# Kernel optimization log

Hardware: AMD Instinct MI355X
Metric: run time of the kernel (lower is better)

Reference implementation:

```python
import jax, jax.numpy as jnp
import numpy as np

B, L, E = 8, 512, 256
H = W = 128
NH = 8
HD = E // NH


def setup_inputs() -> dict:
    key = jax.random.key(0)
    ks = jax.random.split(key, 8)
    return {
        "query_row": jax.random.normal(ks[0], (B, L, E), jnp.float32),
        "query_col": jax.random.normal(ks[1], (B, L, E), jnp.float32),
        "key_row": jax.random.normal(ks[2], (B, H, W, E), jnp.float32),
        "key_col": jax.random.normal(ks[3], (B, H, W, E), jnp.float32),
        "value": jax.random.normal(ks[4], (B, H, W, E), jnp.float32),
        "in_proj_weight": jax.random.normal(ks[5], (5 * E, E), jnp.float32) * 0.02,
        "in_proj_bias": jnp.zeros((5 * E,), jnp.float32),
        "out_proj_weight": jax.random.normal(ks[6], (E, E), jnp.float32) * 0.02,
        "out_proj_bias": jnp.zeros((E,), jnp.float32),
    }


def reference(query_row, query_col, key_row, key_col, value,
              in_proj_weight, in_proj_bias, out_proj_weight, out_proj_bias):
    b, tgt_len, embed_dim = query_row.shape
    h, w = key_col.shape[1], key_row.shape[2]
    nh, hd = NH, embed_dim // NH
    scale = float(hd) ** -0.5

    def proj(x, i):
        Wi = in_proj_weight[i * embed_dim:(i + 1) * embed_dim]
        bi = in_proj_bias[i * embed_dim:(i + 1) * embed_dim]
        return x @ Wi.T + bi

    q_row = proj(query_row, 0) * scale            # [B,L,E]
    q_col = proj(query_col, 1) * scale            # [B,L,E]
    k_row = proj(key_row, 2).mean(axis=1)         # mean over H -> [B,W,E]
    k_col = proj(key_col, 3).mean(axis=2)         # mean over W -> [B,H,E]
    v = proj(value, 4)                            # [B,H,W,E]

    def heads(x):  # [..., E] -> [B, nh, ..., hd]
        return x.reshape(x.shape[:-1] + (nh, hd))

    q_row_h = heads(q_row).transpose(0, 2, 1, 3)        # [B,nh,L,hd]
    q_col_h = heads(q_col).transpose(0, 2, 1, 3)        # [B,nh,L,hd]
    k_row_h = heads(k_row).transpose(0, 2, 1, 3)        # [B,nh,W,hd]
    k_col_h = heads(k_col).transpose(0, 2, 1, 3)        # [B,nh,H,hd]
    v_h = heads(v).transpose(0, 3, 1, 2, 4)             # [B,nh,H,W,hd]

    a_row = jax.nn.softmax(jnp.einsum('bnld,bnwd->bnlw', q_row_h, k_row_h), axis=-1)
    a_col = jax.nn.softmax(jnp.einsum('bnld,bnhd->bnlh', q_col_h, k_col_h), axis=-1)

    # contract over H first, then over W (matches torch's src_len_col >= src_len_row branch)
    ao_col = jnp.einsum('bnlh,bnhwc->bnlwc', a_col, v_h)      # [B,nh,L,W,hd]
    out = jnp.einsum('bnlw,bnlwc->bnlc', a_row, ao_col)       # [B,nh,L,hd]

    out = out.transpose(2, 0, 1, 3).reshape(tgt_len, b, embed_dim)  # [L,B,E]
    return out @ out_proj_weight.T + out_proj_bias
```

## Files before the change

kernel.cpp:

```cpp
#include <hip/hip_runtime.h>
#include <stdint.h>

#define B_  8
#define L_  512
#define E_  256
#define H_  128
#define W_  128
#define NH_ 8
#define HD_ 32

typedef unsigned short ushort_t;
typedef __attribute__((ext_vector_type(8))) short bf16x8;
typedef __attribute__((ext_vector_type(4))) float f32x4;

__device__ __forceinline__ float bf2f(ushort_t u) {
    union { unsigned int i; float f; } x;
    x.i = ((unsigned int)u) << 16;
    return x.f;
}
__device__ __forceinline__ ushort_t f2bf(float f) {
    union { float f; unsigned int i; } x;
    x.f = f;
    unsigned int r = x.i + 0x7FFFu + ((x.i >> 16) & 1u);
    return (ushort_t)(r >> 16);
}

__global__ __launch_bounds__(256) void mean_h_kernel(const float* __restrict__ kr,
                                                     float* __restrict__ out) {
    int i = blockIdx.x * 256 + threadIdx.x;
    int e = i & (E_ - 1);
    int w = (i >> 8) & (W_ - 1);
    int b = i >> 15;
    const float* p = kr + ((size_t)b * H_ * W_ + w) * E_ + e;
    float s = 0.f;
#pragma unroll 8
    for (int h = 0; h < H_; ++h) s += p[(size_t)h * W_ * E_];
    out[i] = s * (1.0f / H_);
}
__global__ __launch_bounds__(256) void mean_w_kernel(const float* __restrict__ kc,
                                                     float* __restrict__ out) {
    int i = blockIdx.x * 256 + threadIdx.x;
    int e = i & (E_ - 1);
    int h = (i >> 8) & (H_ - 1);
    int b = i >> 15;
    const float* p = kc + ((size_t)(b * H_ + h) * W_) * E_ + e;
    float s = 0.f;
#pragma unroll 8
    for (int w = 0; w < W_; ++w) s += p[(size_t)w * E_];
    out[i] = s * (1.0f / W_);
}

__device__ __forceinline__ void load4f(const float* p, float* v) {
    float4 t = *(const float4*)p;
    v[0] = t.x; v[1] = t.y; v[2] = t.z; v[3] = t.w;
}
__device__ __forceinline__ void store4(float* p, float a, float b, float c, float d) {
    float4 t; t.x = a; t.y = b; t.z = c; t.w = d;
    *(float4*)p = t;
}

__global__ __launch_bounds__(256) void gemm256(const float* __restrict__ A,
                                               const float* __restrict__ Wt,
                                               const float* __restrict__ bias,
                                               float* __restrict__ C, int M, float scale) {
    __shared__ __align__(16) float As[16][64];
    __shared__ __align__(16) float Bs[16][64];
    const int m0 = blockIdx.x * 64;
    const int n0 = blockIdx.y * 64;
    const int tid = threadIdx.x;
    const int lr = tid >> 2;
    const int lk = (tid & 3) << 2;
    const int tx = tid & 15, ty = tid >> 4;
    float acc[4][4] = {{0.f}};

    for (int k0 = 0; k0 < E_; k0 += 16) {
        float av[4], wv[4];
        load4f(A + (size_t)(m0 + lr) * E_ + k0 + lk, av);
        load4f(Wt + (size_t)(n0 + lr) * E_ + k0 + lk, wv);
        As[lk + 0][lr] = av[0]; As[lk + 1][lr] = av[1];
        As[lk + 2][lr] = av[2]; As[lk + 3][lr] = av[3];
        Bs[lk + 0][lr] = wv[0]; Bs[lk + 1][lr] = wv[1];
        Bs[lk + 2][lr] = wv[2]; Bs[lk + 3][lr] = wv[3];
        __syncthreads();
#pragma unroll
        for (int k = 0; k < 16; ++k) {
            float a[4], b[4];
            load4f(&As[k][ty << 2], a);
            load4f(&Bs[k][tx << 2], b);
#pragma unroll
            for (int i = 0; i < 4; ++i)
#pragma unroll
                for (int j = 0; j < 4; ++j) acc[i][j] += a[i] * b[j];
        }
        __syncthreads();
    }
    float bv[4];
    load4f(bias + n0 + (tx << 2), bv);
#pragma unroll
    for (int i = 0; i < 4; ++i) {
        float* cp = C + (size_t)(m0 + (ty << 2) + i) * E_ + n0 + (tx << 2);
        store4(cp, scale * (acc[i][0] + bv[0]), scale * (acc[i][1] + bv[1]),
                   scale * (acc[i][2] + bv[2]), scale * (acc[i][3] + bv[3]));
    }
}

__global__ __launch_bounds__(256) void wconv_kernel(const float* __restrict__ w,
                                                    ushort_t* __restrict__ wbf) {
    int i = (blockIdx.x * 256 + threadIdx.x) * 4;
    float4 f = *(const float4*)(w + i);
    ushort4 u;
    u.x = f2bf(f.x); u.y = f2bf(f.y); u.z = f2bf(f.z); u.w = f2bf(f.w);
    *(ushort4*)(wbf + i) = u;
}

#define KP_ 264
__global__ __launch_bounds__(256, 3) void vproj_mfma(const float* __restrict__ Ag,
                                                     const ushort_t* __restrict__ Wbf,
                                                     const float* __restrict__ bias,
                                                     ushort_t* __restrict__ v_t) {
    __shared__ ushort_t A_lds[64 * KP_];
    const int m0 = blockIdx.x * 64;
    const int tid = threadIdx.x, lane = tid & 63, wv = tid >> 6;
    const int quad = lane >> 4, lc = lane & 15;
    {
        int r = tid >> 2, kq = (tid & 3) * 64;
        const float* sa = Ag + (size_t)(m0 + r) * 256 + kq;
        ushort_t* da = A_lds + r * KP_ + kq;
#pragma unroll
        for (int j = 0; j < 16; ++j) {
            float4 f = *(const float4*)(sa + j * 4);
            ushort4 u;
            u.x = f2bf(f.x); u.y = f2bf(f.y); u.z = f2bf(f.z); u.w = f2bf(f.w);
            *(ushort4*)(da + j * 4) = u;
        }
    }
    __syncthreads();

    f32x4 acc[4][4];
#pragma unroll
    for (int t = 0; t < 4; ++t)
#pragma unroll
        for (int et = 0; et < 4; ++et) {
            acc[t][et][0] = 0.f; acc[t][et][1] = 0.f;
            acc[t][et][2] = 0.f; acc[t][et][3] = 0.f;
        }

    const ushort_t* wrow = Wbf + (size_t)(wv * 64 + lc) * 256 + quad * 8;

    bf16x8 wf[4], wn[4];
#pragma unroll
    for (int et = 0; et < 4; ++et)
        wf[et] = *(const bf16x8*)(wrow + (size_t)(et * 16) * 256);

#pragma unroll
    for (int kc = 0; kc < 8; ++kc) {
        bf16x8 vf[4];
#pragma unroll
        for (int t = 0; t < 4; ++t)
            vf[t] = *(const bf16x8*)(A_lds + (t * 16 + lc) * KP_ + kc * 32 + quad * 8);
        if (kc < 7) {
#pragma unroll
            for (int et = 0; et < 4; ++et)
                wn[et] = *(const bf16x8*)(wrow + (size_t)(et * 16) * 256 + (kc + 1) * 32);
        }
#pragma unroll
        for (int et = 0; et < 4; ++et)
#pragma unroll
            for (int t = 0; t < 4; ++t)
                acc[t][et] = __builtin_amdgcn_mfma_f32_16x16x32_bf16(vf[t], wf[et], acc[t][et], 0, 0, 0);
#pragma unroll
        for (int et = 0; et < 4; ++et) wf[et] = wn[et];
    }

    const int b = m0 >> 14;
    const int ml = m0 & 16383;
    ushort_t* vtb = v_t + (size_t)b * 4194304 + ml + quad * 4;
#pragma unroll
    for (int et = 0; et < 4; ++et) {
        const int e = wv * 64 + et * 16 + lc;
        const float bv = bias[e];
        ushort_t* vte = vtb + (size_t)e * 16384;
#pragma unroll
        for (int t = 0; t < 4; ++t) {
            ushort4 u;
            u.x = f2bf(acc[t][et][0] + bv);
            u.y = f2bf(acc[t][et][1] + bv);
            u.z = f2bf(acc[t][et][2] + bv);
            u.w = f2bf(acc[t][et][3] + bv);
            *(ushort4*)(vte + t * 16) = u;
        }
    }
}

__global__ __launch_bounds__(256) void scores_row(const float* __restrict__ q,
                                                  const float* __restrict__ k,
                                                  float* __restrict__ a) {
    const int lt = blockIdx.x, bn = blockIdx.y;
    const int n = bn & 7, b = bn >> 3;
    const int tid = threadIdx.x;
    __shared__ float ks[128][36];
    {
        int r = tid >> 1, c16 = (tid & 1) * 16;
        const float* src = k + ((size_t)b * 128 + r) * 256 + n * 32 + c16;
#pragma unroll
        for (int j = 0; j < 4; ++j) {
            float4 f = *(const float4*)(src + j * 4);
            ks[r][c16 + j * 4 + 0] = f.x; ks[r][c16 + j * 4 + 1] = f.y;
            ks[r][c16 + j * 4 + 2] = f.z; ks[r][c16 + j * 4 + 3] = f.w;
        }
    }
    const int ll = tid >> 3, wq = tid & 7;
    float4 q4r[8];
    {
        const float* qp = q + ((size_t)b * 512 + lt * 32 + ll) * 256 + n * 32;
#pragma unroll
        for (int c4 = 0; c4 < 8; ++c4) q4r[c4] = *(const float4*)(qp + c4 * 4);
    }
    __syncthreads();
    float dots[16];
#pragma unroll
    for (int j = 0; j < 16; ++j) dots[j] = 0.f;
#pragma unroll
    for (int c4 = 0; c4 < 8; ++c4) {
        float4 q4 = q4r[c4];
#pragma unroll
        for (int j = 0; j < 16; ++j) {
            float4 k4 = *(const float4*)&ks[j * 8 + wq][c4 * 4];
            dots[j] += q4.x * k4.x + q4.y * k4.y + q4.z * k4.z + q4.w * k4.w;
        }
    }
    float mx = dots[0];
#pragma unroll
    for (int j = 1; j < 16; ++j) mx = fmaxf(mx, dots[j]);
    for (int d = 1; d < 8; d <<= 1) mx = fmaxf(mx, __shfl_xor(mx, d, 64));
    float ex[16], sm = 0.f;
#pragma unroll
    for (int j = 0; j < 16; ++j) { ex[j] = __expf(dots[j] - mx); sm += ex[j]; }
    for (int d = 1; d < 8; d <<= 1) sm += __shfl_xor(sm, d, 64);
    float inv = 1.0f / sm;
    float* ap = a + ((size_t)bn * 512 + lt * 32 + ll) * 128 + wq;
#pragma unroll
    for (int j = 0; j < 16; ++j) ap[j * 8] = ex[j] * inv;
}

__global__ __launch_bounds__(256) void scores_col(const float* __restrict__ q,
                                                  const float* __restrict__ k,
                                                  float* __restrict__ ac_t) {
    const int lt = blockIdx.x, bn = blockIdx.y;
    const int n = bn & 7, b = bn >> 3;
    const int tid = threadIdx.x;
    __shared__ float qs[32][36];
    __shared__ float sc[128][33];
    __shared__ float mxr[8][32], smr[8][32], fin[2][32];
    {
        int r = tid >> 3, c4 = (tid & 7) * 4;
        float4 f = *(const float4*)(q + ((size_t)b * 512 + lt * 32 + r) * 256 + n * 32 + c4);
        qs[r][c4 + 0] = f.x; qs[r][c4 + 1] = f.y; qs[r][c4 + 2] = f.z; qs[r][c4 + 3] = f.w;
    }
    const int h = tid >> 1, lq = tid & 1;
    float4 kk[8];
    {
        const float* kp = k + ((size_t)b * 128 + h) * 256 + n * 32;
#pragma unroll
        for (int c4 = 0; c4 < 8; ++c4) kk[c4] = *(const float4*)(kp + c4 * 4);
    }
    __syncthreads();
    float dots[16];
#pragma unroll
    for (int j = 0; j < 16; ++j) dots[j] = 0.f;
#pragma unroll
    for (int c4 = 0; c4 < 8; ++c4) {
        float4 k4 = kk[c4];
#pragma unroll
        for (int j = 0; j < 16; ++j) {
            float4 q4 = *(const float4*)&qs[j * 2 + lq][c4 * 4];
            dots[j] += k4.x * q4.x + k4.y * q4.y + k4.z * q4.z + k4.w * q4.w;
        }
    }
#pragma unroll
    for (int j = 0; j < 16; ++j) sc[h][j * 2 + lq] = dots[j];
    __syncthreads();
    {
        int lcol = tid & 31, seg = tid >> 5;
        float m = -3.0e38f;
#pragma unroll
        for (int i = 0; i < 16; ++i) m = fmaxf(m, sc[seg * 16 + i][lcol]);
        mxr[seg][lcol] = m;
    }
    __syncthreads();
    if (tid < 32) {
        float m = mxr[0][tid];
#pragma unroll
        for (int s = 1; s < 8; ++s) m = fmaxf(m, mxr[s][tid]);
        fin[0][tid] = m;
    }
    __syncthreads();
    {
        int lcol = tid & 31, seg = tid >> 5;
        float m = fin[0][lcol], s = 0.f;
#pragma unroll
        for (int i = 0; i < 16; ++i) s += __expf(sc[seg * 16 + i][lcol] - m);
        smr[seg][lcol] = s;
    }
    __syncthreads();
    if (tid < 32) {
        float t = 0.f;
#pragma unroll
        for (int s = 1; s < 8; ++s) t += smr[s][tid];
        fin[1][tid] = 1.0f / (t + smr[0][tid]);
    }
    __syncthreads();
    {
        const int lh = (tid & 1) * 16;
        float* op = ac_t + ((size_t)bn * 128 + h) * 512 + lt * 32;
#pragma unroll
        for (int j4 = 0; j4 < 4; ++j4) {
            int l0 = lh + j4 * 4;
            float4 o;
            o.x = __expf(sc[h][l0 + 0] - fin[0][l0 + 0]) * fin[1][l0 + 0];
            o.y = __expf(sc[h][l0 + 1] - fin[0][l0 + 1]) * fin[1][l0 + 1];
            o.z = __expf(sc[h][l0 + 2] - fin[0][l0 + 2]) * fin[1][l0 + 2];
            o.w = __expf(sc[h][l0 + 3] - fin[0][l0 + 3]) * fin[1][l0 + 3];
            *(float4*)(op + l0) = o;
        }
    }
}

#define ARP 136
#define VBP 136
__global__ __launch_bounds__(256, 3) void core_mfma(const float* __restrict__ a_row,
                                                    const float* __restrict__ ac_t,
                                                    const ushort_t* __restrict__ v_t,
                                                    float* __restrict__ attn) {
    __shared__ ushort_t ar_lds[64 * ARP];
    __shared__ ushort_t vb_lds[2][64 * VBP];
    const int blk = blockIdx.x;
    const int lt = blk >> 6, bn = blk & 63;
    const int n = bn & 7, b = bn >> 3;
    const int tid = threadIdx.x, lane = tid & 63, wv = tid >> 6;
    const int quad = lane >> 4, lc = lane & 15;

    const ushort_t* vtb = v_t + (size_t)b * 4194304 + (size_t)(n * 32) * 16384;
    const int sc_ = tid >> 3, sw = (tid & 7) * 16;

    uint4 p0, p1, p2, p3;
    {
        const ushort_t* s0 = vtb + (size_t)sc_ * 16384 + sw;
        p0 = *(const uint4*)s0;
        p1 = *(const uint4*)(s0 + 8);
        const ushort_t* s1 = s0 + 128;
        p2 = *(const uint4*)s1;
        p3 = *(const uint4*)(s1 + 8);
    }

    {
        const size_t abase = ((size_t)bn * L_ + lt * 64) * 128;
        int r = tid >> 2, wq = (tid & 3) * 32;
        const float* src = a_row + abase + (size_t)r * 128 + wq;
        ushort_t* dst = ar_lds + r * ARP + wq;
#pragma unroll
        for (int j = 0; j < 8; ++j) {
            float4 f = *(const float4*)(src + j * 4);
            ushort4 u;
            u.x = f2bf(f.x); u.y = f2bf(f.y); u.z = f2bf(f.z); u.w = f2bf(f.w);
            *(ushort4*)(dst + j * 4) = u;
        }
    }
    {
        ushort_t* d0 = vb_lds[0] + sc_ * VBP + sw;
        *(uint4*)d0 = p0;
        *(uint4*)(d0 + 8) = p1;
        ushort_t* d1 = d0 + 32 * VBP;
        *(uint4*)d1 = p2;
        *(uint4*)(d1 + 8) = p3;
    }
    __syncthreads();

    const float* act = ac_t + (size_t)bn * 65536 + lt * 64 + wv * 16 + quad * 4;
    bf16x8 A[4];
#pragma unroll
    for (int kc = 0; kc < 4; ++kc)
        A[kc] = *(const bf16x8*)(ar_lds + (wv * 16 + lc) * ARP + kc * 32 + quad * 8);

    f32x4 acc0 = {0.f,0.f,0.f,0.f}, acc1 = {0.f,0.f,0.f,0.f};
    for (int i = 0; i < 64; ++i) {
        const int hh = i * 2, buf = i & 1;
        if (i < 63) {
            const ushort_t* s0 = vtb + (size_t)sc_ * 16384 + (hh + 2) * 128 + sw;
            p0 = *(const uint4*)s0;
            p1 = *(const uint4*)(s0 + 8);
            const ushort_t* s1 = s0 + 128;
            p2 = *(const uint4*)s1;
            p3 = *(const uint4*)(s1 + 8);
        }
        float4 av0 = *(const float4*)(act + (size_t)hh * 512);
        float4 av1 = *(const float4*)(act + (size_t)(hh + 1) * 512);
        const ushort_t* vb0 = vb_lds[buf];
        const ushort_t* vb1 = vb_lds[buf] + 32 * VBP;
        f32x4 t0 = {0.f,0.f,0.f,0.f}, t1 = {0.f,0.f,0.f,0.f};
        f32x4 u0 = {0.f,0.f,0.f,0.f}, u1 = {0.f,0.f,0.f,0.f};
#pragma unroll
        for (int kc = 0; kc < 4; ++kc) {
            const int ko = kc * 32 + quad * 8;
            bf16x8 b0 = *(const bf16x8*)(vb0 + lc * VBP + ko);
            bf16x8 b1 = *(const bf16x8*)(vb0 + (16 + lc) * VBP + ko);
            bf16x8 c0 = *(const bf16x8*)(vb1 + lc * VBP + ko);
            bf16x8 c1 = *(const bf16x8*)(vb1 + (16 + lc) * VBP + ko);
            t0 = __builtin_amdgcn_mfma_f32_16x16x32_bf16(A[kc], b0, t0, 0, 0, 0);
            t1 = __builtin_amdgcn_mfma_f32_16x16x32_bf16(A[kc], b1, t1, 0, 0, 0);
            u0 = __builtin_amdgcn_mfma_f32_16x16x32_bf16(A[kc], c0, u0, 0, 0, 0);
            u1 = __builtin_amdgcn_mfma_f32_16x16x32_bf16(A[kc], c1, u1, 0, 0, 0);
        }
        acc0[0] += av0.x * t0[0] + av1.x * u0[0]; acc1[0] += av0.x * t1[0] + av1.x * u1[0];
        acc0[1] += av0.y * t0[1] + av1.y * u0[1]; acc1[1] += av0.y * t1[1] + av1.y * u1[1];
        acc0[2] += av0.z * t0[2] + av1.z * u0[2]; acc1[2] += av0.z * t1[2] + av1.z * u1[2];
        acc0[3] += av0.w * t0[3] + av1.w * u0[3]; acc1[3] += av0.w * t1[3] + av1.w * u1[3];
        if (i < 63) {
            ushort_t* d0 = vb_lds[buf ^ 1] + sc_ * VBP + sw;
            *(uint4*)d0 = p0;
            *(uint4*)(d0 + 8) = p1;
            ushort_t* d1 = d0 + 32 * VBP;
            *(uint4*)d1 = p2;
            *(uint4*)(d1 + 8) = p3;
            __syncthreads();
        }
    }
    const int row0 = wv * 16 + quad * 4;
#pragma unroll
    for (int r = 0; r < 4; ++r) {
        size_t o = ((size_t)(lt * 64 + row0 + r) * B_ + b) * E_ + n * HD_ + lc;
        attn[o] = acc0[r];
        attn[o + 16] = acc1[r];
    }
}

extern "C" void kernel_launch(void* const* d_in, const int* in_sizes, int n_in,
                              void* d_out, int out_size, void* d_ws, size_t ws_size,
                              hipStream_t stream) {
    const float* query_row = (const float*)d_in[0];
    const float* query_col = (const float*)d_in[1];
    const float* key_row   = (const float*)d_in[2];
    const float* key_col   = (const float*)d_in[3];
    const float* value     = (const float*)d_in[4];
    const float* ipw       = (const float*)d_in[5];
    const float* ipb       = (const float*)d_in[6];
    const float* opw       = (const float*)d_in[7];
    const float* opb       = (const float*)d_in[8];
    float* out = (float*)d_out;

    char* ws = (char*)d_ws;
    float* q_row_s = (float*)ws;  ws += (size_t)4096 * 256 * 4;
    float* q_col_s = (float*)ws;  ws += (size_t)4096 * 256 * 4;
    float* krm     = (float*)ws;  ws += (size_t)262144 * 4;
    float* kcm     = (float*)ws;  ws += (size_t)262144 * 4;
    float* k_row   = (float*)ws;  ws += (size_t)262144 * 4;
    float* k_col   = (float*)ws;  ws += (size_t)262144 * 4;
    ushort_t* v_t  = (ushort_t*)ws; ws += (size_t)33554432 * 2;
    float* a_row   = (float*)ws;  ws += (size_t)4194304 * 4;
    float* ac_t    = (float*)ws;  ws += (size_t)4194304 * 4;
    float* attn    = (float*)ws;  ws += (size_t)4096 * 256 * 4;
    ushort_t* wbf  = (ushort_t*)ws; ws += (size_t)65536 * 2;

    const float scale = 0.17677669529663687f;

    mean_h_kernel<<<1024, 256, 0, stream>>>(key_row, krm);
    mean_w_kernel<<<1024, 256, 0, stream>>>(key_col, kcm);
    wconv_kernel<<<64, 256, 0, stream>>>(ipw + 4 * 65536, wbf);

    gemm256<<<dim3(64, 4), 256, 0, stream>>>(query_row, ipw + 0 * 65536, ipb + 0,    q_row_s, 4096, scale);
    gemm256<<<dim3(64, 4), 256, 0, stream>>>(query_col, ipw + 1 * 65536, ipb + 256,  q_col_s, 4096, scale);
    gemm256<<<dim3(16, 4), 256, 0, stream>>>(krm,       ipw + 2 * 65536, ipb + 512,  k_row,   1024, 1.0f);
    gemm256<<<dim3(16, 4), 256, 0, stream>>>(kcm,       ipw + 3 * 65536, ipb + 768,  k_col,   1024, 1.0f);

    vproj_mfma<<<2048, 256, 0, stream>>>(value, wbf, ipb + 1024, v_t);

    scores_row<<<dim3(16, 64), 256, 0, stream>>>(q_row_s, k_row, a_row);
    scores_col<<<dim3(16, 64), 256, 0, stream>>>(q_col_s, k_col, ac_t);

    core_mfma<<<512, 256, 0, stream>>>(a_row, ac_t, v_t, attn);

    gemm256<<<dim3(64, 4), 256, 0, stream>>>(attn, opw, opb, out, 4096, 1.0f);
}
```

Baseline: 595.0 us.

## Double core kernel L-tile to 128 rows with 512 threads, coalesce fp32 staging loads

The core attention kernel now runs 512-thread blocks covering 128 query rows instead of 64. Each V tile staged in LDS is therefore reused by twice as many rows, which halves V global traffic and the number of blocks. The fp32-to-bf16 staging loops in vproj and core now interleave columns across threads so adjacent lanes read adjacent float4s, giving coalesced loads. vproj occupancy is raised to 4 blocks per SM. The risks are register pressure under the new launch bounds and fewer blocks (256) to fill the GPU.

```diff
diff --git a/kernel.cpp b/kernel.cpp
--- a/kernel.cpp
+++ b/kernel.cpp
@@ -114,7 +114,7 @@
 }
 
 #define KP_ 264
-__global__ __launch_bounds__(256, 3) void vproj_mfma(const float* __restrict__ Ag,
+__global__ __launch_bounds__(256, 4) void vproj_mfma(const float* __restrict__ Ag,
                                                      const ushort_t* __restrict__ Wbf,
                                                      const float* __restrict__ bias,
                                                      ushort_t* __restrict__ v_t) {
@@ -123,15 +123,15 @@
     const int tid = threadIdx.x, lane = tid & 63, wv = tid >> 6;
     const int quad = lane >> 4, lc = lane & 15;
     {
-        int r = tid >> 2, kq = (tid & 3) * 64;
-        const float* sa = Ag + (size_t)(m0 + r) * 256 + kq;
-        ushort_t* da = A_lds + r * KP_ + kq;
+        int r = tid >> 2, c0 = (tid & 3) * 4;
+        const float* sa = Ag + (size_t)(m0 + r) * 256 + c0;
+        ushort_t* da = A_lds + r * KP_ + c0;
 #pragma unroll
         for (int j = 0; j < 16; ++j) {
-            float4 f = *(const float4*)(sa + j * 4);
+            float4 f = *(const float4*)(sa + j * 16);
             ushort4 u;
             u.x = f2bf(f.x); u.y = f2bf(f.y); u.z = f2bf(f.z); u.w = f2bf(f.w);
-            *(ushort4*)(da + j * 4) = u;
+            *(ushort4*)(da + j * 16) = u;
         }
     }
     __syncthreads();
@@ -328,55 +328,49 @@
 
 #define ARP 136
 #define VBP 136
-__global__ __launch_bounds__(256, 3) void core_mfma(const float* __restrict__ a_row,
+__global__ __launch_bounds__(512, 2) void core_mfma(const float* __restrict__ a_row,
                                                     const float* __restrict__ ac_t,
                                                     const ushort_t* __restrict__ v_t,
                                                     float* __restrict__ attn) {
-    __shared__ ushort_t ar_lds[64 * ARP];
+    __shared__ ushort_t ar_lds[128 * ARP];
     __shared__ ushort_t vb_lds[2][64 * VBP];
     const int blk = blockIdx.x;
-    const int lt = blk >> 6, bn = blk & 63;
+    const int ltg = blk >> 6, bn = blk & 63;
     const int n = bn & 7, b = bn >> 3;
     const int tid = threadIdx.x, lane = tid & 63, wv = tid >> 6;
     const int quad = lane >> 4, lc = lane & 15;
 
     const ushort_t* vtb = v_t + (size_t)b * 4194304 + (size_t)(n * 32) * 16384;
-    const int sc_ = tid >> 3, sw = (tid & 7) * 16;
-
-    uint4 p0, p1, p2, p3;
+    const int sc_ = tid >> 4, sw = (tid & 15) * 8;
+
+    uint4 p0, p1;
     {
         const ushort_t* s0 = vtb + (size_t)sc_ * 16384 + sw;
         p0 = *(const uint4*)s0;
-        p1 = *(const uint4*)(s0 + 8);
-        const ushort_t* s1 = s0 + 128;
-        p2 = *(const uint4*)s1;
-        p3 = *(const uint4*)(s1 + 8);
-    }
-
-    {
-        const size_t abase = ((size_t)bn * L_ + lt * 64) * 128;
-        int r = tid >> 2, wq = (tid & 3) * 32;
-        const float* src = a_row + abase + (size_t)r * 128 + wq;
-        ushort_t* dst = ar_lds + r * ARP + wq;
+        p1 = *(const uint4*)(s0 + 128);
+    }
+
+    {
+        const size_t abase = ((size_t)bn * L_ + ltg * 128) * 128;
+        int r = tid >> 2, c0 = (tid & 3) * 4;
+        const float* src = a_row + abase + (size_t)r * 128 + c0;
+        ushort_t* dst = ar_lds + r * ARP + c0;
 #pragma unroll
         for (int j = 0; j < 8; ++j) {
-            float4 f = *(const float4*)(src + j * 4);
+            float4 f = *(const float4*)(src + j * 16);
             ushort4 u;
             u.x = f2bf(f.x); u.y = f2bf(f.y); u.z = f2bf(f.z); u.w = f2bf(f.w);
-            *(ushort4*)(dst + j * 4) = u;
+            *(ushort4*)(dst + j * 16) = u;
         }
     }
     {
         ushort_t* d0 = vb_lds[0] + sc_ * VBP + sw;
         *(uint4*)d0 = p0;
-        *(uint4*)(d0 + 8) = p1;
-        ushort_t* d1 = d0 + 32 * VBP;
-        *(uint4*)d1 = p2;
-        *(uint4*)(d1 + 8) = p3;
-    }
-    __syncthreads();
-
-    const float* act = ac_t + (size_t)bn * 65536 + lt * 64 + wv * 16 + quad * 4;
+        *(uint4*)(d0 + 32 * VBP) = p1;
+    }
+    __syncthreads();
+
+    const float* act = ac_t + (size_t)bn * 65536 + ltg * 128 + wv * 16 + quad * 4;
     bf16x8 A[4];
 #pragma unroll
     for (int kc = 0; kc < 4; ++kc)
@@ -388,10 +382,7 @@
         if (i < 63) {
             const ushort_t* s0 = vtb + (size_t)sc_ * 16384 + (hh + 2) * 128 + sw;
             p0 = *(const uint4*)s0;
-            p1 = *(const uint4*)(s0 + 8);
-            const ushort_t* s1 = s0 + 128;
-            p2 = *(const uint4*)s1;
-            p3 = *(const uint4*)(s1 + 8);
+            p1 = *(const uint4*)(s0 + 128);
         }
         float4 av0 = *(const float4*)(act + (size_t)hh * 512);
         float4 av1 = *(const float4*)(act + (size_t)(hh + 1) * 512);
@@ -418,17 +409,14 @@
         if (i < 63) {
             ushort_t* d0 = vb_lds[buf ^ 1] + sc_ * VBP + sw;
             *(uint4*)d0 = p0;
-            *(uint4*)(d0 + 8) = p1;
-            ushort_t* d1 = d0 + 32 * VBP;
-            *(uint4*)d1 = p2;
-            *(uint4*)(d1 + 8) = p3;
+            *(uint4*)(d0 + 32 * VBP) = p1;
             __syncthreads();
         }
     }
     const int row0 = wv * 16 + quad * 4;
 #pragma unroll
     for (int r = 0; r < 4; ++r) {
-        size_t o = ((size_t)(lt * 64 + row0 + r) * B_ + b) * E_ + n * HD_ + lc;
+        size_t o = ((size_t)(ltg * 128 + row0 + r) * B_ + b) * E_ + n * HD_ + lc;
         attn[o] = acc0[r];
         attn[o + 16] = acc1[r];
     }
@@ -477,7 +465,7 @@
     scores_row<<<dim3(16, 64), 256, 0, stream>>>(q_row_s, k_row, a_row);
     scores_col<<<dim3(16, 64), 256, 0, stream>>>(q_col_s, k_col, ac_t);
 
-    core_mfma<<<512, 256, 0, stream>>>(a_row, ac_t, v_t, attn);
+    core_mfma<<<256, 512, 0, stream>>>(a_row, ac_t, v_t, attn);
 
     gemm256<<<dim3(64, 4), 256, 0, stream>>>(attn, opw, opb, out, 4096, 1.0f);
 }
```

Result: no change. 589.1 us (-1.0%).
